# Optimization experiments

Hardware: AMD Instinct MI355X
Metric: run time of the kernel (lower is better)

## Reference

```python
import jax, jax.numpy as jnp
import numpy as np

N = 100000      # nodes
E = 1600000     # edges (avg degree 16)
F_IN = 128      # dataset.num_features
H = 64          # hidden_channels
C = 40          # dataset.num_classes
LAYERS = 4      # number_conv_layers
EPS = 1e-12     # F.normalize eps


def _agnn_layer(x, src, dst):
    # AGNNConv with beta=1 (requires_grad=False):
    # alpha_ij = softmax_i( cos(x_i, x_j) ), out_i = sum_j alpha_ij * x_j
    xn = x / jnp.maximum(jnp.linalg.norm(x, axis=1, keepdims=True), EPS)
    logits = jnp.sum(xn[dst] * xn[src], axis=1)                      # [E]
    m = jax.lax.stop_gradient(jax.ops.segment_max(logits, dst, num_segments=N))
    e = jnp.exp(logits - m[dst])
    s = jax.ops.segment_sum(e, dst, num_segments=N)
    alpha = e / s[dst]                                               # [E]
    return jax.ops.segment_sum(alpha[:, None] * x[src], dst, num_segments=N)


def setup_inputs() -> dict:
    key = jax.random.key(0)
    k = jax.random.split(key, 6)
    x = jax.random.normal(k[0], (N, F_IN), dtype=jnp.float32)
    edge_index = jax.random.randint(k[1], (2, E), 0, N, dtype=jnp.int32)
    W1 = jax.random.normal(k[2], (F_IN, H), dtype=jnp.float32) * (1.0 / np.sqrt(F_IN))
    b1 = jnp.zeros((H,), dtype=jnp.float32)
    W2 = jax.random.normal(k[3], (H, C), dtype=jnp.float32) * (1.0 / np.sqrt(H))
    b2 = jnp.zeros((C,), dtype=jnp.float32)
    return {"x": x, "W1": W1, "b1": b1, "W2": W2, "b2": b2, "edge_index": edge_index}


def reference(x, W1, b1, W2, b2, edge_index):
    # add self loops (PyG AGNNConv default)
    loop = jnp.arange(N, dtype=edge_index.dtype)
    src = jnp.concatenate([edge_index[0], loop])
    dst = jnp.concatenate([edge_index[1], loop])
    h = jax.nn.relu(x @ W1 + b1)          # lin1 + relu (dropout p=0 / eval)
    for _ in range(LAYERS):
        h = _agnn_layer(h, src, dst)
    out = h @ W2 + b2                     # lin2
    return jax.nn.log_softmax(out, axis=1)
```

## Files before the change

### kernel.cpp

```cpp
#include <hip/hip_runtime.h>
#include <math.h>

#define F_IN 128
#define H_DIM 64
#define C_OUT 40
#define NBK 391
#define CHUNK 4096
#define XPAD 136

typedef _Float16 h8 __attribute__((ext_vector_type(8)));
typedef _Float16 half2t __attribute__((ext_vector_type(2)));
typedef float nf4 __attribute__((ext_vector_type(4)));
typedef _Float16 f16x8 __attribute__((ext_vector_type(8)));
typedef float f32x4 __attribute__((ext_vector_type(4)));

union H8 {
    h8 v;
    half2t p[4];
};

__device__ __forceinline__ float dot8(const H8& a, const H8& b) {
    float d = __builtin_amdgcn_fdot2(a.p[0], b.p[0], 0.0f, false);
    d = __builtin_amdgcn_fdot2(a.p[1], b.p[1], d, false);
    d = __builtin_amdgcn_fdot2(a.p[2], b.p[2], d, false);
    d = __builtin_amdgcn_fdot2(a.p[3], b.p[3], d, false);
    return d;
}


__global__ void __launch_bounds__(256) bhist_kernel(const int* __restrict__ dst,
                                                    int* __restrict__ bhist, int E) {
    __shared__ int lh[512];
    int tid = threadIdx.x;
    lh[tid] = 0; lh[tid + 256] = 0;
    __syncthreads();
    int stride = gridDim.x * 256;
    for (int e = blockIdx.x * 256 + tid; e < E; e += stride) {
        int d = __builtin_nontemporal_load(&dst[e]);
        atomicAdd(&lh[d >> 8], 1);
    }
    __syncthreads();
    if (lh[tid]) atomicAdd(&bhist[tid], lh[tid]);
    if (lh[tid + 256]) atomicAdd(&bhist[tid + 256], lh[tid + 256]);
}

__global__ void __launch_bounds__(512) bscan_kernel(const int* __restrict__ bhist,
                                                    int* __restrict__ bbase,
                                                    int* __restrict__ bcursor, int E) {
    __shared__ int sa[512], sb[512];
    int t = threadIdx.x;
    int v = (t < NBK) ? bhist[t] : 0;
    sa[t] = v;
    __syncthreads();
    int* pa = sa; int* pb = sb;
#pragma unroll
    for (int off = 1; off < 512; off <<= 1) {
        pb[t] = pa[t] + ((t >= off) ? pa[t - off] : 0);
        __syncthreads();
        int* tmp = pa; pa = pb; pb = tmp;
    }
    if (t < NBK) {
        int excl = pa[t] - v;
        bbase[t] = excl;
        bcursor[t] = excl;
    }
    if (t == 0) bbase[NBK] = E;
}

__global__ void __launch_bounds__(256) binscatter_kernel(const int* __restrict__ src,
                                                         const int* __restrict__ dst,
                                                         int* __restrict__ bcursor,
                                                         unsigned int* __restrict__ pairs, int E) {
    __shared__ unsigned int sp[CHUNK];
    __shared__ unsigned short sbof[CHUNK];
    __shared__ int hist[512];
    __shared__ int scanA[512], scanB[512];
    __shared__ int cur[512];
    __shared__ int gbase[512];
    int tid = threadIdx.x;
    int e0 = blockIdx.x * CHUNK;
    int cnt = min(CHUNK, E - e0);

    int dv[CHUNK / 256], sv[CHUNK / 256];
#pragma unroll
    for (int i = 0; i < CHUNK / 256; i++) {
        int idx = tid + i * 256;
        if (idx < cnt) {
            dv[i] = __builtin_nontemporal_load(&dst[e0 + idx]);
            sv[i] = __builtin_nontemporal_load(&src[e0 + idx]);
        }
    }
    hist[tid] = 0; hist[tid + 256] = 0;
    __syncthreads();
#pragma unroll
    for (int i = 0; i < CHUNK / 256; i++) {
        int idx = tid + i * 256;
        if (idx < cnt) atomicAdd(&hist[dv[i] >> 8], 1);
    }
    __syncthreads();
    scanA[tid] = hist[tid]; scanA[tid + 256] = hist[tid + 256];
    __syncthreads();
    int* pa = scanA; int* pb = scanB;
#pragma unroll
    for (int off = 1; off < 512; off <<= 1) {
        pb[tid] = pa[tid] + ((tid >= off) ? pa[tid - off] : 0);
        int t1 = tid + 256;
        pb[t1] = pa[t1] + ((t1 >= off) ? pa[t1 - off] : 0);
        __syncthreads();
        int* tmp = pa; pa = pb; pb = tmp;
    }
    cur[tid] = pa[tid] - hist[tid];
    cur[tid + 256] = pa[tid + 256] - hist[tid + 256];
    __syncthreads();
#pragma unroll
    for (int i = 0; i < CHUNK / 256; i++) {
        int idx = tid + i * 256;
        if (idx < cnt) {
            int b = dv[i] >> 8;
            int lp = atomicAdd(&cur[b], 1);
            sp[lp] = ((unsigned int)(dv[i] & 255) << 24) | (unsigned int)sv[i];
            sbof[lp] = (unsigned short)b;
        }
    }
    {
        int c0 = hist[tid];
        gbase[tid] = c0 ? atomicAdd(&bcursor[tid], c0) : 0;
        int c1 = hist[tid + 256];
        gbase[tid + 256] = c1 ? atomicAdd(&bcursor[tid + 256], c1) : 0;
    }
    __syncthreads();
    for (int i = tid; i < cnt; i += 256) {
        int b = sbof[i];
        int off_in_b = i - (pa[b] - hist[b]);
        pairs[gbase[b] + off_in_b] = sp[i];
    }
}

__global__ void __launch_bounds__(256) bucketsort_kernel(const unsigned int* __restrict__ pairs,
                                                         const int* __restrict__ bbase,
                                                         int* __restrict__ rowptr,
                                                         int* __restrict__ ssrc, int N, int E) {
    __shared__ int hist[256], scanA[256], scanB[256], cur[256];
    int b = blockIdx.x;
    int tid = threadIdx.x;
    int e0 = bbase[b], e1 = bbase[b + 1];
    hist[tid] = 0;
    __syncthreads();
    for (int e = e0 + tid; e < e1; e += 256) {
        unsigned int p = pairs[e];
        atomicAdd(&hist[p >> 24], 1);
    }
    __syncthreads();
    scanA[tid] = hist[tid];
    __syncthreads();
    int* pa = scanA; int* pb = scanB;
#pragma unroll
    for (int off = 1; off < 256; off <<= 1) {
        pb[tid] = pa[tid] + ((tid >= off) ? pa[tid - off] : 0);
        __syncthreads();
        int* tmp = pa; pa = pb; pb = tmp;
    }
    int excl = pa[tid] - hist[tid];
    int node = (b << 8) + tid;
    if (node < N) rowptr[node] = e0 + excl;
    if (b == NBK - 1 && tid == 0) rowptr[N] = E;
    cur[tid] = e0 + excl;
    __syncthreads();
    for (int e = e0 + tid; e < e1; e += 256) {
        unsigned int p = pairs[e];
        int pos = atomicAdd(&cur[p >> 24], 1);
        ssrc[pos] = (int)(p & 0x00FFFFFFu);
    }
}

__global__ void __launch_bounds__(256) cvtw_kernel(const float* __restrict__ W1,
                                                   _Float16* __restrict__ w1t) {
    int t = blockIdx.x * 256 + threadIdx.x;
    if (t < F_IN * H_DIM) {
        int k = t >> 6, col = t & 63;
        w1t[col * F_IN + k] = (_Float16)W1[t];
    }
}

__global__ void __launch_bounds__(256) lin1_kernel(
        const float* __restrict__ x, const _Float16* __restrict__ w1t,
        const float* __restrict__ b1, _Float16* __restrict__ hnout,
        float* __restrict__ nrmout, int n) {
    __shared__ _Float16 sx[64 * XPAD];
    __shared__ _Float16 sw[64 * XPAD];
    int tid = threadIdx.x;
    int r0 = blockIdx.x * 64;

    for (int ch = tid; ch < 64 * 32; ch += 256) {
        int row = ch >> 5, k4 = (ch & 31) << 2;
        float4 xv = make_float4(0.f, 0.f, 0.f, 0.f);
        if (r0 + row < n) xv = *(const float4*)(x + (size_t)(r0 + row) * F_IN + k4);
        _Float16* p = &sx[row * XPAD + k4];
        p[0] = (_Float16)xv.x; p[1] = (_Float16)xv.y;
        p[2] = (_Float16)xv.z; p[3] = (_Float16)xv.w;
    }
    for (int ch = tid; ch < 64 * 16; ch += 256) {
        int col = ch >> 4, k8 = (ch & 15) << 3;
        *(uint4*)&sw[col * XPAD + k8] = *(const uint4*)(w1t + col * F_IN + k8);
    }
    __syncthreads();

    int w = tid >> 6, lane = tid & 63;
    int q = lane >> 4, c = lane & 15;

    f16x8 afrag[4];
#pragma unroll
    for (int kk = 0; kk < 4; kk++)
        afrag[kk] = *(const f16x8*)&sx[(w * 16 + c) * XPAD + kk * 32 + q * 8];

    f32x4 acc[4] = {{0.f,0.f,0.f,0.f},{0.f,0.f,0.f,0.f},{0.f,0.f,0.f,0.f},{0.f,0.f,0.f,0.f}};
#pragma unroll
    for (int ct = 0; ct < 4; ct++) {
#pragma unroll
        for (int kk = 0; kk < 4; kk++) {
            f16x8 bfrag = *(const f16x8*)&sw[(ct * 16 + c) * XPAD + kk * 32 + q * 8];
            acc[ct] = __builtin_amdgcn_mfma_f32_16x16x32_f16(afrag[kk], bfrag, acc[ct], 0, 0, 0);
        }
    }

    float ss[4] = {0.f, 0.f, 0.f, 0.f};
#pragma unroll
    for (int ct = 0; ct < 4; ct++) {
        float bv = b1[ct * 16 + c];
#pragma unroll
        for (int r = 0; r < 4; r++) {
            float v = fmaxf(acc[ct][r] + bv, 0.0f);
            acc[ct][r] = v;
            ss[r] = fmaf(v, v, ss[r]);
        }
    }
#pragma unroll
    for (int k = 1; k < 16; k <<= 1) {
#pragma unroll
        for (int r = 0; r < 4; r++) ss[r] += __shfl_xor(ss[r], k, 64);
    }
    float nn[4], inv[4];
#pragma unroll
    for (int r = 0; r < 4; r++) {
        nn[r] = fmaxf(sqrtf(ss[r]), 1e-12f);
        inv[r] = 1.0f / nn[r];
    }
#pragma unroll
    for (int ct = 0; ct < 4; ct++)
#pragma unroll
        for (int r = 0; r < 4; r++)
            sx[(w * 16 + q * 4 + r) * XPAD + ct * 16 + c] = (_Float16)(acc[ct][r] * inv[r]);

    if (c == 0) {
#pragma unroll
        for (int r = 0; r < 4; r++) {
            int row = r0 + w * 16 + q * 4 + r;
            if (row < n) nrmout[row] = nn[r];
        }
    }
#pragma unroll
    for (int it = 0; it < 2; it++) {
        int row = w * 16 + it * 8 + (lane >> 3);
        int k8 = (lane & 7) * 8;
        if (r0 + row < n)
            *(uint4*)(hnout + (size_t)(r0 + row) * H_DIM + k8) =
                *(const uint4*)&sx[row * XPAD + k8];
    }
}

__global__ void __launch_bounds__(256) agnn_kernel(
        const h8* __restrict__ h, const float* __restrict__ nrm,
        const int* __restrict__ rowptr, const int* __restrict__ ssrc,
        h8* __restrict__ hout, float* __restrict__ nrmout, int n) {
    int wid = (blockIdx.x * blockDim.x + threadIdx.x) >> 6;
    int t = threadIdx.x & 63;
    if (wid >= n) return;
    int g = t >> 3;
    int sub = t & 7;

    H8 hd; hd.v = h[(size_t)wid * 8 + sub];
    float ni = nrm[wid];

    int e0 = rowptr[wid];
    int end = rowptr[wid + 1];
    int deg = end - e0;
    int base = e0 + g;

    bool v0 = base < end;
    bool v1 = base + 8 < end;
    int s0 = 0, s1 = 0;
    if (v0) s0 = ssrc[base];
    if (v1) s1 = ssrc[base + 8];
    H8 A, B;
    A.v = (h8)(_Float16)0; B.v = (h8)(_Float16)0;
    float n0 = 0.f, n1 = 0.f;
    if (v0) { A.v = h[(size_t)s0 * 8 + sub]; n0 = nrm[s0]; }
    if (v1) { B.v = h[(size_t)s1 * 8 + sub]; n1 = nrm[s1]; }

    bool big = deg > 16;
    H8 C, D;
    C.v = (h8)(_Float16)0; D.v = (h8)(_Float16)0;
    float n2 = 0.f, n3 = 0.f;
    bool v2 = false, v3 = false;
    if (big) {
        v2 = base + 16 < end;
        v3 = base + 24 < end;
        int s2 = 0, s3 = 0;
        if (v2) s2 = ssrc[base + 16];
        if (v3) s3 = ssrc[base + 24];
        if (v2) { C.v = h[(size_t)s2 * 8 + sub]; n2 = nrm[s2]; }
        if (v3) { D.v = h[(size_t)s3 * 8 + sub]; n3 = nrm[s3]; }
    }

    float dself = dot8(hd, hd);
#pragma unroll
    for (int k = 1; k < 8; k <<= 1) dself += __shfl_xor(dself, k, 64);
    float wself = __expf(dself);
    float aself = wself * ni;

    half2t acc2[4];
    float sw;
    if (g == 0) {
        half2t ap = {(_Float16)aself, (_Float16)aself};
#pragma unroll
        for (int j = 0; j < 4; j++) acc2[j] = ap * hd.p[j];
        sw = wself;
    } else {
        half2t z = {(_Float16)0.0f, (_Float16)0.0f};
#pragma unroll
        for (int j = 0; j < 4; j++) acc2[j] = z;
        sw = 0.0f;
    }

    {
        float d0 = dot8(A, hd);
        float d1 = dot8(B, hd);
#pragma unroll
        for (int k = 1; k < 8; k <<= 1) {
            d0 += __shfl_xor(d0, k, 64);
            d1 += __shfl_xor(d1, k, 64);
        }
        float w0 = v0 ? __expf(d0) : 0.0f;
        float w1 = v1 ? __expf(d1) : 0.0f;
        sw += w0 + w1;
        float a0 = w0 * n0;
        float a1 = w1 * n1;
        half2t a0p = {(_Float16)a0, (_Float16)a0};
        half2t a1p = {(_Float16)a1, (_Float16)a1};
#pragma unroll
        for (int j = 0; j < 4; j++) acc2[j] += a0p * A.p[j] + a1p * B.p[j];
    }
    if (big) {
        float d2 = dot8(C, hd);
        float d3 = dot8(D, hd);
#pragma unroll
        for (int k = 1; k < 8; k <<= 1) {
            d2 += __shfl_xor(d2, k, 64);
            d3 += __shfl_xor(d3, k, 64);
        }
        float w2 = v2 ? __expf(d2) : 0.0f;
        float w3 = v3 ? __expf(d3) : 0.0f;
        sw += w2 + w3;
        float a2 = w2 * n2;
        float a3 = w3 * n3;
        half2t a2p = {(_Float16)a2, (_Float16)a2};
        half2t a3p = {(_Float16)a3, (_Float16)a3};
#pragma unroll
        for (int j = 0; j < 4; j++) acc2[j] += a2p * C.p[j] + a3p * D.p[j];
    }

    for (int e = base + 32; e < end; e += 8) {
        int st = ssrc[e];
        H8 T;
        T.v = h[(size_t)st * 8 + sub];
        float nt = nrm[st];
        float dt = dot8(T, hd);
#pragma unroll
        for (int k = 1; k < 8; k <<= 1) dt += __shfl_xor(dt, k, 64);
        float wt = __expf(dt);
        sw += wt;
        float at = wt * nt;
        half2t atp = {(_Float16)at, (_Float16)at};
#pragma unroll
        for (int j = 0; j < 4; j++) acc2[j] += atp * T.p[j];
    }

#pragma unroll
    for (int k = 8; k < 64; k <<= 1) {
#pragma unroll
        for (int j = 0; j < 4; j++) {
            int u = __shfl_xor(__builtin_bit_cast(int, acc2[j]), k, 64);
            acc2[j] += __builtin_bit_cast(half2t, u);
        }
        sw += __shfl_xor(sw, k, 64);
    }

    float inv = 1.0f / sw;
    float o[8];
#pragma unroll
    for (int j = 0; j < 4; j++) {
        o[2 * j] = (float)acc2[j][0] * inv;
        o[2 * j + 1] = (float)acc2[j][1] * inv;
    }
    float ss = 0.0f;
#pragma unroll
    for (int i = 0; i < 8; i++) ss = fmaf(o[i], o[i], ss);
#pragma unroll
    for (int k = 1; k < 8; k <<= 1) ss += __shfl_xor(ss, k, 64);
    float nn = fmaxf(sqrtf(ss), 1e-12f);
    if (g == 0) {
        float r = 1.0f / nn;
        h8 oh;
#pragma unroll
        for (int i = 0; i < 8; i++) oh[i] = (_Float16)(o[i] * r);
        hout[(size_t)wid * 8 + sub] = oh;
    }
    if (t == 0) nrmout[wid] = nn;
}

__global__ void __launch_bounds__(256) lin2_kernel(
        const h8* __restrict__ h, const float* __restrict__ nrm,
        const float* __restrict__ W2, const float* __restrict__ b2,
        float* __restrict__ out, int n) {
    __shared__ h8 sh[32 * 8];
    __shared__ float snrm[32];
    int tid = threadIdx.x;
    int r0 = blockIdx.x * 32;
    int rows = min(32, n - r0);

    {
        const uint4* hg = (const uint4*)(h + (size_t)r0 * 8);
        uint4* sh4 = (uint4*)sh;
        int tot = rows * 8;
        for (int i = tid; i < tot; i += 256) sh4[i] = hg[i];
        if (tid < rows) snrm[tid] = nrm[r0 + tid];
    }
    __syncthreads();

    int wave = tid >> 6, lane = tid & 63;
    int rbase = wave * 8;

    float acc[8];
    if (lane < C_OUT) {
#pragma unroll
        for (int j = 0; j < 8; j++) acc[j] = 0.0f;
#pragma unroll 2
        for (int k = 0; k < H_DIM; k += 8) {
            float w[8];
#pragma unroll
            for (int i = 0; i < 8; i++) w[i] = W2[(k + i) * C_OUT + lane];
#pragma unroll
            for (int j = 0; j < 8; j++) {
                h8 hv = sh[(rbase + j) * 8 + (k >> 3)];
#pragma unroll
                for (int i = 0; i < 8; i++) acc[j] = fmaf((float)hv[i], w[i], acc[j]);
            }
        }
        float bl = b2[lane];
#pragma unroll
        for (int j = 0; j < 8; j++) acc[j] = fmaf(snrm[rbase + j], acc[j], bl);
    } else {
#pragma unroll
        for (int j = 0; j < 8; j++) acc[j] = -INFINITY;
    }

#pragma unroll
    for (int j = 0; j < 8; j++) {
        int r = rbase + j;
        if (r >= rows) break;
        float m = acc[j];
#pragma unroll
        for (int k = 1; k < 64; k <<= 1) m = fmaxf(m, __shfl_xor(m, k, 64));
        float e = (lane < C_OUT) ? __expf(acc[j] - m) : 0.0f;
        float s = e;
#pragma unroll
        for (int k = 1; k < 64; k <<= 1) s += __shfl_xor(s, k, 64);
        if (lane < C_OUT) out[(size_t)(r0 + r) * C_OUT + lane] = acc[j] - m - logf(s);
    }
}


extern "C" void kernel_launch(void* const* d_in, const int* in_sizes, int n_in,
                              void* d_out, int out_size, void* d_ws, size_t ws_size,
                              hipStream_t stream) {
    const float* x = (const float*)d_in[0];
    const float* W1 = (const float*)d_in[1];
    const float* b1 = (const float*)d_in[2];
    const float* W2 = (const float*)d_in[3];
    const float* b2 = (const float*)d_in[4];
    const int* ei = (const int*)d_in[5];

    const int N = in_sizes[0] / F_IN;
    const int E = in_sizes[5] / 2;
    const int* src = ei;
    const int* dst = ei + E;

    char* w = (char*)d_ws;
    auto carve = [&](size_t bytes) {
        char* p = w;
        w += (bytes + 255) & ~(size_t)255;
        return p;
    };
    _Float16* g1 = (_Float16*)carve((size_t)N * H_DIM * 2);
    _Float16* g2 = (_Float16*)carve((size_t)N * H_DIM * 2);
    float* rn1 = (float*)carve((size_t)N * 4);
    float* rn2 = (float*)carve((size_t)N * 4);
    int* rowptr = (int*)carve((size_t)(N + 1) * 4);
    int* bhist = (int*)carve(512 * 4);
    int* bbase = (int*)carve(512 * 4);
    int* bcursor = (int*)carve(512 * 4);
    int* ssrc = (int*)carve((size_t)E * 4);
    _Float16* w1t = (_Float16*)carve((size_t)F_IN * H_DIM * 2);
    unsigned int* pairs = (unsigned int*)g2;

    (void)hipMemsetAsync(bhist, 0, 512 * 4, stream);
    bhist_kernel<<<512, 256, 0, stream>>>(dst, bhist, E);
    bscan_kernel<<<1, 512, 0, stream>>>(bhist, bbase, bcursor, E);
    binscatter_kernel<<<(E + CHUNK - 1) / CHUNK, 256, 0, stream>>>(src, dst, bcursor, pairs, E);
    bucketsort_kernel<<<NBK, 256, 0, stream>>>(pairs, bbase, rowptr, ssrc, N, E);

    cvtw_kernel<<<(F_IN * H_DIM + 255) / 256, 256, 0, stream>>>(W1, w1t);
    lin1_kernel<<<(N + 63) / 64, 256, 0, stream>>>(x, w1t, b1, g1, rn1, N);

    {
        int blocks = (N * 64 + 255) / 256;
        agnn_kernel<<<blocks, 256, 0, stream>>>((const h8*)g1, rn1, rowptr, ssrc, (h8*)g2, rn2, N);
        agnn_kernel<<<blocks, 256, 0, stream>>>((const h8*)g2, rn2, rowptr, ssrc, (h8*)g1, rn1, N);
        agnn_kernel<<<blocks, 256, 0, stream>>>((const h8*)g1, rn1, rowptr, ssrc, (h8*)g2, rn2, N);
        agnn_kernel<<<blocks, 256, 0, stream>>>((const h8*)g2, rn2, rowptr, ssrc, (h8*)g1, rn1, N);
    }

    lin2_kernel<<<(N + 31) / 32, 256, 0, stream>>>((const h8*)g1, rn1, W2, b2, (float*)d_out, N);
}
```

Before: 299.6 us.

## Map 8 nodes per wavefront with 8-lane groups and DPP reductions

Each AGNN layer now gives each destination node an 8-lane group instead of a whole 64-lane wavefront. Each group walks that node's edges four at a time, so the cross-group shuffle reduction of accumulators is no longer needed. The 8-lane dot-product and norm reductions use DPP row operations instead of ds_swizzle/shfl. The aim is to cut reduction overhead and raise edge-level parallelism per wave. The cost is intra-wave load imbalance: every wave loops to the maximum degree of its 8 nodes, and fewer independent loads are in flight per node.

```diff
diff --git a/kernel.cpp b/kernel.cpp
--- a/kernel.cpp
+++ b/kernel.cpp
@@ -25,6 +25,16 @@
     d = __builtin_amdgcn_fdot2(a.p[2], b.p[2], d, false);
     d = __builtin_amdgcn_fdot2(a.p[3], b.p[3], d, false);
     return d;
+}
+
+__device__ __forceinline__ float dpp_red8_add(float x) {
+    int v = __builtin_bit_cast(int, x);
+    x += __builtin_bit_cast(float, __builtin_amdgcn_update_dpp(0, v, 0xB1, 0xF, 0xF, true));
+    v = __builtin_bit_cast(int, x);
+    x += __builtin_bit_cast(float, __builtin_amdgcn_update_dpp(0, v, 0x4E, 0xF, 0xF, true));
+    v = __builtin_bit_cast(int, x);
+    x += __builtin_bit_cast(float, __builtin_amdgcn_update_dpp(0, v, 0x141, 0xF, 0xF, true));
+    return x;
 }
 
 
@@ -272,127 +282,72 @@
         const h8* __restrict__ h, const float* __restrict__ nrm,
         const int* __restrict__ rowptr, const int* __restrict__ ssrc,
         h8* __restrict__ hout, float* __restrict__ nrmout, int n) {
-    int wid = (blockIdx.x * blockDim.x + threadIdx.x) >> 6;
-    int t = threadIdx.x & 63;
-    if (wid >= n) return;
-    int g = t >> 3;
-    int sub = t & 7;
-
-    H8 hd; hd.v = h[(size_t)wid * 8 + sub];
-    float ni = nrm[wid];
-
-    int e0 = rowptr[wid];
-    int end = rowptr[wid + 1];
-    int deg = end - e0;
-    int base = e0 + g;
-
-    bool v0 = base < end;
-    bool v1 = base + 8 < end;
-    int s0 = 0, s1 = 0;
-    if (v0) s0 = ssrc[base];
-    if (v1) s1 = ssrc[base + 8];
-    H8 A, B;
-    A.v = (h8)(_Float16)0; B.v = (h8)(_Float16)0;
-    float n0 = 0.f, n1 = 0.f;
-    if (v0) { A.v = h[(size_t)s0 * 8 + sub]; n0 = nrm[s0]; }
-    if (v1) { B.v = h[(size_t)s1 * 8 + sub]; n1 = nrm[s1]; }
-
-    bool big = deg > 16;
-    H8 C, D;
-    C.v = (h8)(_Float16)0; D.v = (h8)(_Float16)0;
-    float n2 = 0.f, n3 = 0.f;
-    bool v2 = false, v3 = false;
-    if (big) {
-        v2 = base + 16 < end;
-        v3 = base + 24 < end;
-        int s2 = 0, s3 = 0;
-        if (v2) s2 = ssrc[base + 16];
-        if (v3) s3 = ssrc[base + 24];
+    int wv = (blockIdx.x * blockDim.x + threadIdx.x) >> 6;
+    int lane = threadIdx.x & 63;
+    int g = lane >> 3;
+    int sub = lane & 7;
+    int wid = wv * 8 + g;
+    bool nvalid = wid < n;
+    int nid = nvalid ? wid : (n - 1);
+
+    int e0 = rowptr[nid];
+    int e1 = rowptr[nid + 1];
+    int steps = nvalid ? (e1 - e0) : 0;
+
+    H8 hd; hd.v = h[(size_t)nid * 8 + sub];
+    float ni = nrm[nid];
+
+    int mx = steps;
+    mx = max(mx, __shfl_xor(mx, 8, 64));
+    mx = max(mx, __shfl_xor(mx, 16, 64));
+    mx = max(mx, __shfl_xor(mx, 32, 64));
+
+    float dself = dpp_red8_add(dot8(hd, hd));
+    float wself = __expf(dself);
+    float sw = wself;
+    float aself = wself * ni;
+    half2t ap = {(_Float16)aself, (_Float16)aself};
+    half2t acc2[4];
+#pragma unroll
+    for (int j = 0; j < 4; j++) acc2[j] = ap * hd.p[j];
+
+    for (int it = 0; it < mx; it += 4) {
+        bool v0 = it < steps;
+        bool v1 = it + 1 < steps;
+        bool v2 = it + 2 < steps;
+        bool v3 = it + 3 < steps;
+        int s0 = 0, s1 = 0, s2 = 0, s3 = 0;
+        if (v0) s0 = ssrc[e0 + it];
+        if (v1) s1 = ssrc[e0 + it + 1];
+        if (v2) s2 = ssrc[e0 + it + 2];
+        if (v3) s3 = ssrc[e0 + it + 3];
+        H8 A, B, C, D;
+        A.v = (h8)(_Float16)0; B.v = (h8)(_Float16)0;
+        C.v = (h8)(_Float16)0; D.v = (h8)(_Float16)0;
+        float n0 = 0.f, n1 = 0.f, n2 = 0.f, n3 = 0.f;
+        if (v0) { A.v = h[(size_t)s0 * 8 + sub]; n0 = nrm[s0]; }
+        if (v1) { B.v = h[(size_t)s1 * 8 + sub]; n1 = nrm[s1]; }
         if (v2) { C.v = h[(size_t)s2 * 8 + sub]; n2 = nrm[s2]; }
         if (v3) { D.v = h[(size_t)s3 * 8 + sub]; n3 = nrm[s3]; }
-    }
-
-    float dself = dot8(hd, hd);
-#pragma unroll
-    for (int k = 1; k < 8; k <<= 1) dself += __shfl_xor(dself, k, 64);
-    float wself = __expf(dself);
-    float aself = wself * ni;
-
-    half2t acc2[4];
-    float sw;
-    if (g == 0) {
-        half2t ap = {(_Float16)aself, (_Float16)aself};
-#pragma unroll
-        for (int j = 0; j < 4; j++) acc2[j] = ap * hd.p[j];
-        sw = wself;
-    } else {
-        half2t z = {(_Float16)0.0f, (_Float16)0.0f};
-#pragma unroll
-        for (int j = 0; j < 4; j++) acc2[j] = z;
-        sw = 0.0f;
-    }
-
-    {
-        float d0 = dot8(A, hd);
-        float d1 = dot8(B, hd);
-#pragma unroll
-        for (int k = 1; k < 8; k <<= 1) {
-            d0 += __shfl_xor(d0, k, 64);
-            d1 += __shfl_xor(d1, k, 64);
-        }
+
+        float d0 = dpp_red8_add(dot8(A, hd));
+        float d1 = dpp_red8_add(dot8(B, hd));
+        float d2 = dpp_red8_add(dot8(C, hd));
+        float d3 = dpp_red8_add(dot8(D, hd));
+
         float w0 = v0 ? __expf(d0) : 0.0f;
         float w1 = v1 ? __expf(d1) : 0.0f;
-        sw += w0 + w1;
-        float a0 = w0 * n0;
-        float a1 = w1 * n1;
+        float w2 = v2 ? __expf(d2) : 0.0f;
+        float w3 = v3 ? __expf(d3) : 0.0f;
+        sw += (w0 + w1) + (w2 + w3);
+        float a0 = w0 * n0, a1 = w1 * n1, a2 = w2 * n2, a3 = w3 * n3;
         half2t a0p = {(_Float16)a0, (_Float16)a0};
         half2t a1p = {(_Float16)a1, (_Float16)a1};
-#pragma unroll
-        for (int j = 0; j < 4; j++) acc2[j] += a0p * A.p[j] + a1p * B.p[j];
-    }
-    if (big) {
-        float d2 = dot8(C, hd);
-        float d3 = dot8(D, hd);
-#pragma unroll
-        for (int k = 1; k < 8; k <<= 1) {
-            d2 += __shfl_xor(d2, k, 64);
-            d3 += __shfl_xor(d3, k, 64);
-        }
-        float w2 = v2 ? __expf(d2) : 0.0f;
-        float w3 = v3 ? __expf(d3) : 0.0f;
-        sw += w2 + w3;
-        float a2 = w2 * n2;
-        float a3 = w3 * n3;
         half2t a2p = {(_Float16)a2, (_Float16)a2};
         half2t a3p = {(_Float16)a3, (_Float16)a3};
 #pragma unroll
-        for (int j = 0; j < 4; j++) acc2[j] += a2p * C.p[j] + a3p * D.p[j];
-    }
-
-    for (int e = base + 32; e < end; e += 8) {
-        int st = ssrc[e];
-        H8 T;
-        T.v = h[(size_t)st * 8 + sub];
-        float nt = nrm[st];
-        float dt = dot8(T, hd);
-#pragma unroll
-        for (int k = 1; k < 8; k <<= 1) dt += __shfl_xor(dt, k, 64);
-        float wt = __expf(dt);
-        sw += wt;
-        float at = wt * nt;
-        half2t atp = {(_Float16)at, (_Float16)at};
-#pragma unroll
-        for (int j = 0; j < 4; j++) acc2[j] += atp * T.p[j];
-    }
-
-#pragma unroll
-    for (int k = 8; k < 64; k <<= 1) {
-#pragma unroll
-        for (int j = 0; j < 4; j++) {
-            int u = __shfl_xor(__builtin_bit_cast(int, acc2[j]), k, 64);
-            acc2[j] += __builtin_bit_cast(half2t, u);
-        }
-        sw += __shfl_xor(sw, k, 64);
+        for (int j = 0; j < 4; j++)
+            acc2[j] += a0p * A.p[j] + a1p * B.p[j] + a2p * C.p[j] + a3p * D.p[j];
     }
 
     float inv = 1.0f / sw;
@@ -405,17 +360,16 @@
     float ss = 0.0f;
 #pragma unroll
     for (int i = 0; i < 8; i++) ss = fmaf(o[i], o[i], ss);
-#pragma unroll
-    for (int k = 1; k < 8; k <<= 1) ss += __shfl_xor(ss, k, 64);
+    ss = dpp_red8_add(ss);
     float nn = fmaxf(sqrtf(ss), 1e-12f);
-    if (g == 0) {
-        float r = 1.0f / nn;
-        h8 oh;
-#pragma unroll
-        for (int i = 0; i < 8; i++) oh[i] = (_Float16)(o[i] * r);
+    float r = 1.0f / nn;
+    h8 oh;
+#pragma unroll
+    for (int i = 0; i < 8; i++) oh[i] = (_Float16)(o[i] * r);
+    if (nvalid) {
         hout[(size_t)wid * 8 + sub] = oh;
-    }
-    if (t == 0) nrmout[wid] = nn;
+        if (sub == 0) nrmout[wid] = nn;
+    }
 }
 
 __global__ void __launch_bounds__(256) lin2_kernel(
@@ -523,7 +477,7 @@
     lin1_kernel<<<(N + 63) / 64, 256, 0, stream>>>(x, w1t, b1, g1, rn1, N);
 
     {
-        int blocks = (N * 64 + 255) / 256;
+        int blocks = (N + 31) / 32;
         agnn_kernel<<<blocks, 256, 0, stream>>>((const h8*)g1, rn1, rowptr, ssrc, (h8*)g2, rn2, N);
         agnn_kernel<<<blocks, 256, 0, stream>>>((const h8*)g2, rn2, rowptr, ssrc, (h8*)g1, rn1, N);
         agnn_kernel<<<blocks, 256, 0, stream>>>((const h8*)g1, rn1, rowptr, ssrc, (h8*)g2, rn2, N);
```

After: 265.2 us. -11.5%, faster.
